# Performance work log

Hardware: AMD Instinct MI355X
Metric: run time of the kernel (lower is better)

The kernel has to match this reference:

```python
import jax, jax.numpy as jnp
import numpy as np


def setup_inputs() -> dict:
    key = jax.random.key(0)
    k1, k2 = jax.random.split(key)
    B, t, nbands, framesize = 32, 4000, 65, 80
    H = jax.random.normal(k1, (B, t, nbands), dtype=jnp.float32)
    noise = jax.random.uniform(k2, (B, t, framesize), dtype=jnp.float32)  # uniform [0,1); scaled to [-1,1) in reference
    return {"H": H, "noise": noise, "framesize": framesize}


def reference(H, noise, framesize):
    # H: [B, t, nbands] real half-spectrum of zero-phase filter
    B, t, nbands = H.shape
    L_fir = 2 * nbands - 1  # FIR length (129)

    # zero-phase impulse response -> linear-phase via circular shift
    zero_phase = jnp.fft.irfft(H, n=L_fir, axis=-1)          # [B, t, L_fir]
    lin_phase = jnp.roll(zero_phase, nbands - 1, axis=-1)

    # periodic Hann window (matches torch.hann_window default periodic=True)
    n = jnp.arange(L_fir, dtype=H.dtype)
    hann = 0.5 * (1.0 - jnp.cos(2.0 * jnp.pi * n / L_fir))
    firwin = lin_phase * hann                                 # [B, t, L_fir]

    # per-frame noise in [-1, 1)
    x = noise * 2.0 - 1.0                                     # [B, t, framesize]

    # full FFT convolution along last axis
    L = framesize + L_fir - 1                                 # 208
    X = jnp.fft.rfft(x, n=L, axis=-1)
    W = jnp.fft.rfft(firwin, n=L, axis=-1)
    filtered = jnp.fft.irfft(X * W, n=L, axis=-1)             # [B, t, L]

    # overlap-add with hop = framesize via scatter-add (replaces conv_transpose1d trick)
    total = (t - 1) * framesize + L
    idx = jnp.arange(t)[:, None] * framesize + jnp.arange(L)[None, :]  # [t, L]
    out = jnp.zeros((B, total), dtype=filtered.dtype).at[:, idx].add(filtered)

    # trim filter group delay from both ends -> [B, t*framesize]
    return out[:, nbands - 1: total - (nbands - 1)]
```

## Files before the change

kernel.cpp:

```cpp
#include <hip/hip_runtime.h>


#define NT 256
#define X_STRIDE 84
#define W_STRIDE 158
#define W_P 14
#define NSLOT 35
#define WTOT_H 5536
#define HF_STRIDE 104
#define UTOT_F 2496

typedef _Float16 f16x8 __attribute__((ext_vector_type(8)));
typedef _Float16 f16x4 __attribute__((ext_vector_type(4)));
typedef _Float16 h2 __attribute__((ext_vector_type(2)));
typedef float f32x4 __attribute__((ext_vector_type(4)));

union U32H2 { unsigned u; h2 h; };
static __device__ __forceinline__ h2 swap_h2(h2 v) {
  U32H2 a; a.h = v;
  U32H2 o; o.u = __builtin_amdgcn_alignbit(a.u, a.u, 16);
  return o.h;
}
static __device__ __forceinline__ h2 mid_h2(h2 lo, h2 hi) {
  U32H2 a, b; a.h = lo; b.h = hi;
  U32H2 o; o.u = __builtin_amdgcn_alignbit(b.u, a.u, 16);
  return o.h;
}

__global__ void __launch_bounds__(256)
minit_kernel(_Float16* __restrict__ M) {
  const float TP = 6.28318530717958647692f / 129.f;
  int i = blockIdx.x * 256 + threadIdx.x;
  int frag = i >> 9;
  int off  = i & 511;
  int lane = off >> 3, j = off & 7;
  int nt = frag / 3, ks = frag - 3 * (frag / 3);
  int n = nt * 16 + (lane & 15);
  int k = ks * 32 + (lane >> 4) * 8 + j;
  float v = 0.f;
  if (n <= 128 && k <= 64) {
    float hann = 0.5f - 0.5f * __cosf((float)n * TP);
    float sc = (k == 0 ? 1.f : 2.f) * (1.f / 129.f);
    int e = (k * (n - 64)) % 129; if (e < 0) e += 129;
    v = hann * sc * __cosf((float)e * TP);
  }
  M[i] = (_Float16)v;
}

__global__ void __launch_bounds__(NT)
fng_kernel(const float* __restrict__ Hg_, const float* __restrict__ Ng_,
           float* __restrict__ Og_, const _Float16* __restrict__ Mg) {
  __shared__ __align__(16) _Float16 sWh[WTOT_H];
  __shared__ __align__(16) float sU[UTOT_F];

  const int t  = threadIdx.x;
  const int bx = blockIdx.x;
  const int b  = blockIdx.y;
  const int f0 = bx * 32;

  float4 xq[3];
  {
    float4 z4 = {0.f, 0.f, 0.f, 0.f};
    for (int i = t; i < WTOT_H / 8; i += NT) ((float4*)sWh)[i] = z4;
    _Float16* sHf = (_Float16*)sU;
    const float* Hg = Hg_ + (size_t)b * (4000 * 65);
    for (int i = t; i < 48 * 96; i += NT) {
      int row = i / 96, k = i - 96 * (i / 96);
      int fr = f0 - 2 + row;
      float v = 0.f;
      if (k < 65 && row < NSLOT && fr >= 0 && fr < 4000) v = Hg[fr * 65 + k];
      sHf[row * HF_STRIDE + k] = (_Float16)v;
    }
    const float* Ng = Ng_ + (size_t)b * 320000;
#pragma unroll
    for (int j = 0; j < 3; ++j) {
      int q = t + 256 * j;
      float4 v = {0.5f, 0.5f, 0.5f, 0.5f};
      if (q < NSLOT * 21) {
        int fi = q / 21, qm = q - fi * 21;
        int fr = f0 - 2 + fi;
        if (qm < 20 && fr >= 0 && fr < 4000)
          v = *(const float4*)&Ng[(size_t)fr * 80 + 4 * qm];
      }
      xq[j] = v;
    }
  }
  __syncthreads();

  {
    const _Float16* sHf = (const _Float16*)sU;
    const int wv   = t >> 6;
    const int lane = t & 63;
    const int quad = lane >> 4;
    const int l15  = lane & 15;
#pragma unroll 1
    for (int tile = wv; tile < 27; tile += 4) {
      const int mt = tile / 9, nt = tile - 9 * (tile / 9);
      f32x4 acc = {0.f, 0.f, 0.f, 0.f};
#pragma unroll
      for (int ks = 0; ks < 3; ++ks) {
        f16x8 a = *(const f16x8*)&sHf[(mt * 16 + l15) * HF_STRIDE + ks * 32 + quad * 8];
        f16x8 bb = ((const f16x8*)Mg)[(nt * 3 + ks) * 64 + lane];
        acc = __builtin_amdgcn_mfma_f32_16x16x32_f16(a, bb, acc, 0, 0, 0);
      }
      const int n = nt * 16 + l15;
      const int fr0 = mt * 16 + quad * 4;
      if (n <= 128) {
#pragma unroll
        for (int r = 0; r < 4; ++r) {
          int frame = fr0 + r;
          if (frame < NSLOT) sWh[frame * W_STRIDE + W_P + n] = (_Float16)acc[r];
        }
      }
    }
  }
  __syncthreads();

  {
    _Float16* sXh = (_Float16*)sU;
#pragma unroll
    for (int j = 0; j < 3; ++j) {
      int q = t + 256 * j;
      if (q < NSLOT * 21) {
        int fi = q / 21, qm = q - fi * 21;
        if (qm < 20) {
          float4 v = xq[j];
          f16x4 o;
          o.x = (_Float16)(2.f * v.x - 1.f); o.y = (_Float16)(2.f * v.y - 1.f);
          o.z = (_Float16)(2.f * v.z - 1.f); o.w = (_Float16)(2.f * v.w - 1.f);
          *(f16x4*)&sXh[fi * X_STRIDE + 4 * qm] = o;
        }
      }
    }
  }
  __syncthreads();

  {
    const _Float16* sXh = (const _Float16*)sU;
    const int col = t & 31;
    const int pb  = t >> 5;
    const int e   = 64 + 10 * pb;
    const int qq  = (e >= 80) ? 1 : 0;
    const int D   = e - 80 * qq;
    float acc[10];
#pragma unroll
    for (int i = 0; i < 10; ++i) acc[i] = 0.f;

#pragma unroll 1
    for (int g = 2; g >= -1; --g) {
      const int dlt = D + 80 * g;
      int Qlo = (dlt - 131 + 3) >> 2; if (Qlo < 0) Qlo = 0;
      int Qhi = (dlt + 9) >> 2;       if (Qhi > 19) Qhi = 19;
      if (Qlo > Qhi) continue;
      const int slot = col + qq - g + 2;
      const _Float16* wr = &sWh[slot * W_STRIDE];
      const _Float16* xr = &sXh[slot * X_STRIDE];
      int wb = W_P + dlt - 4 * Qlo - 4;

      h2 wE[7], wO[6];
#pragma unroll
      for (int k = 0; k < 7; ++k) wE[k] = *(const h2*)&wr[wb + 2 * k];
#pragma unroll
      for (int k = 0; k < 6; ++k) wO[k] = mid_h2(wE[k], wE[k + 1]);

#define PAIR(K) (((K) & 1) ? wO[((K) - 1) >> 1] : wE[(K) >> 1])
#pragma unroll 4
      for (int Q = Qlo; Q <= Qhi; ++Q) {
        f16x4 x4 = *(const f16x4*)&xr[4 * Q];
        h2 x01; x01.x = x4.x; x01.y = x4.y;
        h2 x23; x23.x = x4.z; x23.y = x4.w;
        h2 xs01 = swap_h2(x01);
        h2 xs23 = swap_h2(x23);
#pragma unroll
        for (int i = 0; i < 10; ++i) {
          acc[i] = __builtin_amdgcn_fdot2(xs01, PAIR(i + 3), acc[i], false);
          acc[i] = __builtin_amdgcn_fdot2(xs23, PAIR(i + 1), acc[i], false);
        }
        wb -= 4; int wc = (wb < 0) ? 0 : wb;
#pragma unroll
        for (int k = 6; k >= 2; --k) wE[k] = wE[k - 2];
#pragma unroll
        for (int k = 5; k >= 2; --k) wO[k] = wO[k - 2];
        wE[0] = *(const h2*)&wr[wc];
        wE[1] = *(const h2*)&wr[wc + 2];
        wO[0] = mid_h2(wE[0], wE[1]);
        wO[1] = mid_h2(wE[1], wE[2]);
      }
#undef PAIR
    }

    float* Ob = Og_ + (size_t)b * 320000 + 2560 * bx + 80 * col + 10 * pb;
#pragma unroll
    for (int s = 0; s < 5; ++s) {
      float2 v; v.x = acc[2 * s]; v.y = acc[2 * s + 1];
      *(float2*)&Ob[2 * s] = v;
    }
  }
}

extern "C" void kernel_launch(void* const* d_in, const int* in_sizes, int n_in,
                              void* d_out, int out_size, void* d_ws, size_t ws_size,
                              hipStream_t stream) {
  const float* H     = (const float*)d_in[0];
  const float* noise = (const float*)d_in[1];
  float* out = (float*)d_out;
  _Float16* M = (_Float16*)d_ws;
  (void)in_sizes; (void)n_in; (void)ws_size; (void)out_size;

  minit_kernel<<<54, 256, 0, stream>>>(M);
  dim3 grid(125, 32, 1);
  fng_kernel<<<grid, NT, 0, stream>>>(H, noise, out, M);
}
```

Baseline: 171.1 us.

## Store noise reversed in LDS, unroll conv inner loop by 8 taps, drop a barrier

Noise is loaded, scaled and stored to LDS in reversed order, so the per-pair half swaps in the convolution loop go away. H and X get separate LDS buffers, which removes the register staging of the noise and one __syncthreads. The direct-convolution loop now handles 8 input samples per iteration with a wider sliding window of filter taps, which cuts loop overhead and window-shift work per tap. The cost is more register pressure from the larger tap window and more LDS.

Result: no change. 168.2 us (-1.6%).

```diff
diff --git a/kernel.cpp b/kernel.cpp
--- a/kernel.cpp
+++ b/kernel.cpp
@@ -4,11 +4,12 @@
 #define NT 256
 #define X_STRIDE 84
 #define W_STRIDE 158
-#define W_P 14
+#define W_P 18
 #define NSLOT 35
-#define WTOT_H 5536
+#define WTOT_H 5544
 #define HF_STRIDE 104
-#define UTOT_F 2496
+#define HTOT_H 4992
+#define XTOT_H 2940
 
 typedef _Float16 f16x8 __attribute__((ext_vector_type(8)));
 typedef _Float16 f16x4 __attribute__((ext_vector_type(4)));
@@ -16,11 +17,6 @@
 typedef float f32x4 __attribute__((ext_vector_type(4)));
 
 union U32H2 { unsigned u; h2 h; };
-static __device__ __forceinline__ h2 swap_h2(h2 v) {
-  U32H2 a; a.h = v;
-  U32H2 o; o.u = __builtin_amdgcn_alignbit(a.u, a.u, 16);
-  return o.h;
-}
 static __device__ __forceinline__ h2 mid_h2(h2 lo, h2 hi) {
   U32H2 a, b; a.h = lo; b.h = hi;
   U32H2 o; o.u = __builtin_amdgcn_alignbit(b.u, a.u, 16);
@@ -51,44 +47,68 @@
 fng_kernel(const float* __restrict__ Hg_, const float* __restrict__ Ng_,
            float* __restrict__ Og_, const _Float16* __restrict__ Mg) {
   __shared__ __align__(16) _Float16 sWh[WTOT_H];
-  __shared__ __align__(16) float sU[UTOT_F];
+  __shared__ __align__(16) _Float16 sXh[XTOT_H];
+  __shared__ __align__(16) _Float16 sHf[HTOT_H];
 
   const int t  = threadIdx.x;
   const int bx = blockIdx.x;
   const int b  = blockIdx.y;
   const int f0 = bx * 32;
 
-  float4 xq[3];
   {
     float4 z4 = {0.f, 0.f, 0.f, 0.f};
     for (int i = t; i < WTOT_H / 8; i += NT) ((float4*)sWh)[i] = z4;
-    _Float16* sHf = (_Float16*)sU;
+  }
+
+  {
     const float* Hg = Hg_ + (size_t)b * (4000 * 65);
-    for (int i = t; i < 48 * 96; i += NT) {
-      int row = i / 96, k = i - 96 * (i / 96);
-      int fr = f0 - 2 + row;
-      float v = 0.f;
-      if (k < 65 && row < NSLOT && fr >= 0 && fr < 4000) v = Hg[fr * 65 + k];
-      sHf[row * HF_STRIDE + k] = (_Float16)v;
-    }
+#pragma unroll
+    for (int j = 0; j < 4; ++j) {
+      int i = t + NT * j;
+      if (i < 35 * 24) {
+        int r = i / 24, u = i - 24 * r;
+        int fr = f0 - 2 + r;
+        f16x4 o = {(_Float16)0.f, (_Float16)0.f, (_Float16)0.f, (_Float16)0.f};
+        if (u < 16) {
+          if (fr >= 0 && fr < 4000) {
+            const float* hp = &Hg[fr * 65 + 4 * u];
+            o.x = (_Float16)hp[0]; o.y = (_Float16)hp[1];
+            o.z = (_Float16)hp[2]; o.w = (_Float16)hp[3];
+          }
+          *(f16x4*)&sHf[r * HF_STRIDE + 4 * u] = o;
+        } else if (u == 16) {
+          if (fr >= 0 && fr < 4000) o.x = (_Float16)Hg[fr * 65 + 64];
+          *(f16x4*)&sHf[r * HF_STRIDE + 64] = o;
+        } else {
+          *(f16x4*)&sHf[r * HF_STRIDE + 4 * u] = o;
+        }
+      }
+    }
+  }
+
+  {
     const float* Ng = Ng_ + (size_t)b * 320000;
 #pragma unroll
     for (int j = 0; j < 3; ++j) {
-      int q = t + 256 * j;
-      float4 v = {0.5f, 0.5f, 0.5f, 0.5f};
-      if (q < NSLOT * 21) {
-        int fi = q / 21, qm = q - fi * 21;
+      int q = t + NT * j;
+      if (q < NSLOT * 20) {
+        int fi = q / 20, qm = q - 20 * fi;
         int fr = f0 - 2 + fi;
-        if (qm < 20 && fr >= 0 && fr < 4000)
-          v = *(const float4*)&Ng[(size_t)fr * 80 + 4 * qm];
-      }
-      xq[j] = v;
+        f16x4 o = {(_Float16)0.f, (_Float16)0.f, (_Float16)0.f, (_Float16)0.f};
+        if (fr >= 0 && fr < 4000) {
+          float4 v = *(const float4*)&Ng[(size_t)fr * 80 + 4 * qm];
+          o.x = (_Float16)(2.f * v.w - 1.f);
+          o.y = (_Float16)(2.f * v.z - 1.f);
+          o.z = (_Float16)(2.f * v.y - 1.f);
+          o.w = (_Float16)(2.f * v.x - 1.f);
+        }
+        *(f16x4*)&sXh[fi * X_STRIDE + (76 - 4 * qm)] = o;
+      }
     }
   }
   __syncthreads();
 
   {
-    const _Float16* sHf = (const _Float16*)sU;
     const int wv   = t >> 6;
     const int lane = t & 63;
     const int quad = lane >> 4;
@@ -117,26 +137,6 @@
   __syncthreads();
 
   {
-    _Float16* sXh = (_Float16*)sU;
-#pragma unroll
-    for (int j = 0; j < 3; ++j) {
-      int q = t + 256 * j;
-      if (q < NSLOT * 21) {
-        int fi = q / 21, qm = q - fi * 21;
-        if (qm < 20) {
-          float4 v = xq[j];
-          f16x4 o;
-          o.x = (_Float16)(2.f * v.x - 1.f); o.y = (_Float16)(2.f * v.y - 1.f);
-          o.z = (_Float16)(2.f * v.z - 1.f); o.w = (_Float16)(2.f * v.w - 1.f);
-          *(f16x4*)&sXh[fi * X_STRIDE + 4 * qm] = o;
-        }
-      }
-    }
-  }
-  __syncthreads();
-
-  {
-    const _Float16* sXh = (const _Float16*)sU;
     const int col = t & 31;
     const int pb  = t >> 5;
     const int e   = 64 + 10 * pb;
@@ -149,44 +149,56 @@
 #pragma unroll 1
     for (int g = 2; g >= -1; --g) {
       const int dlt = D + 80 * g;
-      int Qlo = (dlt - 131 + 3) >> 2; if (Qlo < 0) Qlo = 0;
-      int Qhi = (dlt + 9) >> 2;       if (Qhi > 19) Qhi = 19;
-      if (Qlo > Qhi) continue;
+      int Ulo = (dlt - 128) >> 3; if (Ulo < 0) Ulo = 0;
+      int Uhi = (dlt + 9) >> 3;   if (Uhi > 9) Uhi = 9;
+      if (Ulo > Uhi) continue;
       const int slot = col + qq - g + 2;
       const _Float16* wr = &sWh[slot * W_STRIDE];
       const _Float16* xr = &sXh[slot * X_STRIDE];
-      int wb = W_P + dlt - 4 * Qlo - 4;
-
-      h2 wE[7], wO[6];
-#pragma unroll
-      for (int k = 0; k < 7; ++k) wE[k] = *(const h2*)&wr[wb + 2 * k];
-#pragma unroll
-      for (int k = 0; k < 6; ++k) wO[k] = mid_h2(wE[k], wE[k + 1]);
-
-#define PAIR(K) (((K) & 1) ? wO[((K) - 1) >> 1] : wE[(K) >> 1])
+      int wb = W_P + dlt - 8 * Ulo - 4;
+
+      h2 wEa[10], wOa[9];
+#pragma unroll
+      for (int k2 = 0; k2 < 10; ++k2) wEa[k2] = *(const h2*)&wr[wb - 4 + 2 * k2];
+#pragma unroll
+      for (int k2 = 0; k2 < 9; ++k2) wOa[k2] = mid_h2(wEa[k2], wEa[k2 + 1]);
+
+#define PAIRX(K) (((K) & 1) ? wOa[(((K) - 1) >> 1) + 2] : wEa[(((K) >> 1) + 2)])
 #pragma unroll 4
-      for (int Q = Qlo; Q <= Qhi; ++Q) {
-        f16x4 x4 = *(const f16x4*)&xr[4 * Q];
-        h2 x01; x01.x = x4.x; x01.y = x4.y;
-        h2 x23; x23.x = x4.z; x23.y = x4.w;
-        h2 xs01 = swap_h2(x01);
-        h2 xs23 = swap_h2(x23);
+      for (int U = Ulo; U <= Uhi; ++U) {
+        const _Float16* xp = &xr[72 - 8 * U];
+        f16x4 q0 = *(const f16x4*)&xp[0];
+        f16x4 q1 = *(const f16x4*)&xp[4];
+        h2 xD; xD.x = q0.x; xD.y = q0.y;
+        h2 xC; xC.x = q0.z; xC.y = q0.w;
+        h2 xB; xB.x = q1.x; xB.y = q1.y;
+        h2 xA; xA.x = q1.z; xA.y = q1.w;
 #pragma unroll
         for (int i = 0; i < 10; ++i) {
-          acc[i] = __builtin_amdgcn_fdot2(xs01, PAIR(i + 3), acc[i], false);
-          acc[i] = __builtin_amdgcn_fdot2(xs23, PAIR(i + 1), acc[i], false);
-        }
-        wb -= 4; int wc = (wb < 0) ? 0 : wb;
-#pragma unroll
-        for (int k = 6; k >= 2; --k) wE[k] = wE[k - 2];
-#pragma unroll
-        for (int k = 5; k >= 2; --k) wO[k] = wO[k - 2];
-        wE[0] = *(const h2*)&wr[wc];
-        wE[1] = *(const h2*)&wr[wc + 2];
-        wO[0] = mid_h2(wE[0], wE[1]);
-        wO[1] = mid_h2(wE[1], wE[2]);
-      }
-#undef PAIR
+          float a = acc[i];
+          a = __builtin_amdgcn_fdot2(xA, PAIRX(i + 3), a, false);
+          a = __builtin_amdgcn_fdot2(xB, PAIRX(i + 1), a, false);
+          a = __builtin_amdgcn_fdot2(xC, PAIRX(i - 1), a, false);
+          a = __builtin_amdgcn_fdot2(xD, PAIRX(i - 3), a, false);
+          acc[i] = a;
+        }
+        int wl = wb - 12; if (wl < 0) wl = 0;
+        const _Float16* wp = &wr[wl];
+#pragma unroll
+        for (int k2 = 9; k2 >= 4; --k2) wEa[k2] = wEa[k2 - 4];
+#pragma unroll
+        for (int k2 = 8; k2 >= 4; --k2) wOa[k2] = wOa[k2 - 4];
+        wEa[0] = *(const h2*)&wp[0];
+        wEa[1] = *(const h2*)&wp[2];
+        wEa[2] = *(const h2*)&wp[4];
+        wEa[3] = *(const h2*)&wp[6];
+        wOa[0] = mid_h2(wEa[0], wEa[1]);
+        wOa[1] = mid_h2(wEa[1], wEa[2]);
+        wOa[2] = mid_h2(wEa[2], wEa[3]);
+        wOa[3] = mid_h2(wEa[3], wEa[4]);
+        wb -= 8;
+      }
+#undef PAIRX
     }
 
     float* Ob = Og_ + (size_t)b * 320000 + 2560 * bx + 80 * col + 10 * pb;
```
